# Performance work log

Hardware: AMD Instinct MI355X
Metric: run time of the kernel (lower is better)

## Reference

```python
import jax, jax.numpy as jnp
import numpy as np

LAYERS = [3, 1024, 512, 256, 128, 1]
WIDTHS = [3, 1024, 1024, 1024, 1024, 1]  # width per BsPINN: 2^(i-1)*Layers[i]
N = 131072


def _mask(num_blocks, bs1, bs2):
    # block-diagonal mask of ones, built statically (constant under jit)
    return jnp.asarray(np.kron(np.eye(num_blocks, dtype=np.float32),
                               np.ones((bs1, bs2), dtype=np.float32)))


def _xavier(key, shape, fan_in, fan_out):
    lim = np.sqrt(6.0 / (fan_in + fan_out)).astype(np.float32)
    return jax.random.uniform(key, shape, jnp.float32, -lim, lim)


def setup_inputs() -> dict:
    key = jax.random.key(0)
    ks = jax.random.split(key, 6)
    inp = {
        "X": jax.random.uniform(ks[0], (N, 3), dtype=jnp.float32),
        "lb_X": jnp.zeros((3,), jnp.float32),
        "ub_X": jnp.ones((3,), jnp.float32),
    }
    for i in range(5):
        # xavier scale per sub-block Layers[i] x Layers[i+1], as in the torch init
        inp[f"W{i}"] = _xavier(ks[i + 1], (WIDTHS[i], WIDTHS[i + 1]),
                               LAYERS[i], LAYERS[i + 1])
        inp[f"b{i}"] = jnp.zeros((1, WIDTHS[i + 1]), jnp.float32)
    return inp


def reference(X, lb_X, ub_X, W0, b0, W1, b1, W2, b2, W3, b3, W4, b4):
    # masks for hidden layers l=2,3: 2 blocks of 512x512, 4 blocks of 256x256
    m2 = _mask(2, LAYERS[2], 2 * LAYERS[3])   # [1024,1024]
    m3 = _mask(4, LAYERS[3], 2 * LAYERS[4])   # [1024,1024]
    h = 2.0 * (X - lb_X) / (ub_X - lb_X) - 1.0  # [N,3]
    h = jnp.sin(h @ W0 + b0)            # [N,1024] dense
    h = jnp.sin(h @ W1 + b1)            # [N,1024] dense
    h = jnp.sin(h @ (W2 * m2) + b2)     # [N,1024] block-diag (2 blocks)
    h = jnp.sin(h @ (W3 * m3) + b3)     # [N,1024] block-diag (4 blocks)
    return h @ W4 + b4                  # [N,1]
```

## Files before the change

### kernel.cpp

```cpp
#include <hip/hip_runtime.h>

typedef _Float16 f16x8 __attribute__((ext_vector_type(8)));
typedef _Float16 f16x4 __attribute__((ext_vector_type(4)));
typedef __fp16  fp16x2 __attribute__((ext_vector_type(2)));
typedef float f32x4 __attribute__((ext_vector_type(4)));
typedef unsigned int u32;

#define ROWS 64
#define THREADS 512

__global__ __launch_bounds__(512) void pack_weights(
    const float* __restrict__ W1, const float* __restrict__ W2,
    const float* __restrict__ W3, _Float16* __restrict__ WF1,
    _Float16* __restrict__ WF2, _Float16* __restrict__ WF3) {
  int t = blockIdx.x * 512 + threadIdx.x;
  const float* src; _Float16* dst; int idx, ct, kt, lane, kbase;
  if (t < 131072) {
    idx = t; src = W1; dst = WF1;
    ct = idx >> 11; kt = (idx >> 6) & 31; lane = idx & 63; kbase = 0;
  } else if (t < 196608) {
    idx = t - 131072; src = W2; dst = WF2;
    ct = idx >> 10; kt = (idx >> 6) & 15; lane = idx & 63;
    kbase = (ct >= 32) ? 512 : 0;
  } else {
    idx = t - 196608; src = W3; dst = WF3;
    ct = idx >> 9; kt = (idx >> 6) & 7; lane = idx & 63;
    kbase = (ct >> 4) << 8;
  }
  int c  = ct * 16 + (lane & 15);
  int k0 = kbase + kt * 32 + ((lane >> 4) << 3);
  f16x8 v;
#pragma unroll
  for (int j = 0; j < 8; ++j) v[j] = (_Float16)src[(size_t)(k0 + j) * 1024 + c];
  *reinterpret_cast<f16x8*>(dst + (size_t)idx * 8) = v;
}

template <int KT>
__device__ __forceinline__ void layer_mfma(char* hb, const _Float16* __restrict__ WF,
                                           const float* __restrict__ bias,
                                           int wid, int lane, int kbase) {
  f32x4 acc[8][4];
#pragma unroll
  for (int cf = 0; cf < 8; ++cf)
#pragma unroll
    for (int rf = 0; rf < 4; ++rf) acc[cf][rf] = f32x4{0.f, 0.f, 0.f, 0.f};

  const f16x8* wf = reinterpret_cast<const f16x8*>(WF) +
                    (u32)(wid * 8 * KT * 64 + lane);
  const int arow = lane & 15;
  const int koff = (lane >> 4) << 3;
  const u32 abase = (u32)(arow * 2048);
  const u32 axor  = (u32)((arow & 7) << 4);

  f16x8 wA[8], wB[8];
#define LOADW(buf, ktv)                                                        \
  { u32 _kt = (u32)(ktv);                                                      \
    _Pragma("unroll") for (int cf = 0; cf < 8; ++cf)                           \
      buf[cf] = wf[(u32)(cf * KT) * 64u + _kt * 64u]; }
#define DOMFMA(w, ktv)                                                         \
  { u32 kb = (u32)((kbase + (ktv) * 32 + koff) * 2);                           \
    f16x8 h[4];                                                                \
    _Pragma("unroll") for (int rf = 0; rf < 4; ++rf) {                         \
      u32 addr = ((u32)(rf * 32768) + abase + kb) ^ axor;                      \
      h[rf] = *reinterpret_cast<const f16x8*>(hb + addr);                      \
    }                                                                          \
    __builtin_amdgcn_s_setprio(1);                                             \
    _Pragma("unroll") for (int cf = 0; cf < 8; ++cf)                           \
      _Pragma("unroll") for (int rf = 0; rf < 4; ++rf)                         \
        acc[cf][rf] = __builtin_amdgcn_mfma_f32_16x16x32_f16(w[cf], h[rf],     \
                                                             acc[cf][rf], 0, 0, 0); \
    __builtin_amdgcn_s_setprio(0); }

  LOADW(wA, 0);
#pragma unroll 1
  for (int kt = 0; kt < KT; kt += 2) {
    int ktn = (kt + 2 < KT) ? (kt + 2) : 0;
    LOADW(wB, kt + 1);
    DOMFMA(wA, kt);
    LOADW(wA, ktn);
    DOMFMA(wB, kt + 1);
  }
#undef LOADW
#undef DOMFMA

  __syncthreads();
  const int csub = (lane >> 4) << 2;
  const int rr   = lane & 15;
#pragma unroll
  for (int cf = 0; cf < 8; ++cf) {
    int c0 = wid * 128 + cf * 16 + csub;
    f32x4 bb = *reinterpret_cast<const f32x4*>(bias + c0);
#pragma unroll
    for (int rf = 0; rf < 4; ++rf) {
      int r = rf * 16 + rr;
      float s0 = __sinf(acc[cf][rf][0] + bb[0]);
      float s1 = __sinf(acc[cf][rf][1] + bb[1]);
      float s2 = __sinf(acc[cf][rf][2] + bb[2]);
      float s3 = __sinf(acc[cf][rf][3] + bb[3]);
      union { fp16x2 h2[2]; f16x4 v; } pk;
      pk.h2[0] = __builtin_amdgcn_cvt_pkrtz(s0, s1);
      pk.h2[1] = __builtin_amdgcn_cvt_pkrtz(s2, s3);
      u32 addr = ((u32)(r * 2048 + c0 * 2)) ^ ((u32)((r & 7) << 4));
      *reinterpret_cast<f16x4*>(hb + addr) = pk.v;
    }
  }
  __syncthreads();
}

__global__
__attribute__((amdgpu_flat_work_group_size(512, 512), amdgpu_waves_per_eu(2, 2)))
void bspinn_fused(
    const float* __restrict__ X, const float* __restrict__ lb,
    const float* __restrict__ ub,
    const float* __restrict__ W0, const float* __restrict__ b0,
    const _Float16* __restrict__ WF1, const float* __restrict__ b1,
    const _Float16* __restrict__ WF2, const float* __restrict__ b2,
    const _Float16* __restrict__ WF3, const float* __restrict__ b3,
    const float* __restrict__ W4, const float* __restrict__ b4,
    float* __restrict__ out) {
  __shared__ alignas(16) char hb[ROWS * 2048];
  __shared__ float xs[ROWS * 4];
  __shared__ float partials[ROWS * 8];

  const int tid  = threadIdx.x;
  const int lane = tid & 63;
  const int wid  = tid >> 6;
  const int r0   = blockIdx.x * ROWS;

  if (tid < ROWS * 3) {
    int r = tid / 3, j = tid - r * 3;
    float x = X[(size_t)r0 * 3 + tid];
    xs[r * 4 + j] = 2.0f * (x - lb[j]) / (ub[j] - lb[j]) - 1.0f;
  }
  __syncthreads();

  {
    int c0 = tid * 2;
    float wa0 = W0[c0],        wb0 = W0[c0 + 1];
    float wa1 = W0[1024 + c0], wb1 = W0[1025 + c0];
    float wa2 = W0[2048 + c0], wb2 = W0[2049 + c0];
    float ba = b0[c0], bbv = b0[c0 + 1];
#pragma unroll 4
    for (int r = 0; r < ROWS; ++r) {
      float x0 = xs[r * 4], x1 = xs[r * 4 + 1], x2 = xs[r * 4 + 2];
      float va = __sinf(fmaf(x2, wa2, fmaf(x1, wa1, fmaf(x0, wa0, ba))));
      float vb = __sinf(fmaf(x2, wb2, fmaf(x1, wb1, fmaf(x0, wb0, bbv))));
      union { fp16x2 h2; u32 u; } pk;
      pk.h2 = __builtin_amdgcn_cvt_pkrtz(va, vb);
      u32 addr = ((u32)(r * 2048 + c0 * 2)) ^ ((u32)((r & 7) << 4));
      *reinterpret_cast<u32*>(hb + addr) = pk.u;
    }
  }
  __syncthreads();

  layer_mfma<32>(hb, WF1, b1, wid, lane, 0);
  layer_mfma<16>(hb, WF2, b2, wid, lane, (wid >> 2) * 512);
  layer_mfma<8 >(hb, WF3, b3, wid, lane, (wid >> 1) * 256);

  {
    int r = lane, seg = wid;
    u32 rb = (u32)(r * 2048);
    u32 xr = (u32)((r & 7) << 4);
    float s = 0.f;
#pragma unroll
    for (int kk = 0; kk < 128; kk += 8) {
      int k = seg * 128 + kk;
      f16x8 v = *reinterpret_cast<const f16x8*>(hb + ((rb + (u32)(k * 2)) ^ xr));
#pragma unroll
      for (int j = 0; j < 8; ++j) s = fmaf((float)v[j], W4[k + j], s);
    }
    partials[seg * 64 + r] = s;
  }
  __syncthreads();
  if (tid < ROWS) {
    float s = b4[0];
#pragma unroll
    for (int g = 0; g < 8; ++g) s += partials[g * 64 + tid];
    out[r0 + tid] = s;
  }
}

extern "C" void kernel_launch(void* const* d_in, const int* in_sizes, int n_in,
                              void* d_out, int out_size, void* d_ws, size_t ws_size,
                              hipStream_t stream) {
  const float* X  = (const float*)d_in[0];
  const float* lb = (const float*)d_in[1];
  const float* ub = (const float*)d_in[2];
  const float* W0 = (const float*)d_in[3];
  const float* b0 = (const float*)d_in[4];
  const float* W1 = (const float*)d_in[5];
  const float* b1 = (const float*)d_in[6];
  const float* W2 = (const float*)d_in[7];
  const float* b2 = (const float*)d_in[8];
  const float* W3 = (const float*)d_in[9];
  const float* b3 = (const float*)d_in[10];
  const float* W4 = (const float*)d_in[11];
  const float* b4 = (const float*)d_in[12];
  float* out = (float*)d_out;

  _Float16* WF1 = (_Float16*)d_ws;
  _Float16* WF2 = (_Float16*)((char*)d_ws + 2097152);
  _Float16* WF3 = (_Float16*)((char*)d_ws + 2097152 + 1048576);

  hipLaunchKernelGGL(pack_weights, dim3(448), dim3(512), 0, stream,
                     W1, W2, W3, WF1, WF2, WF3);
  hipLaunchKernelGGL(bspinn_fused, dim3(131072 / ROWS), dim3(THREADS), 0, stream,
                     X, lb, ub, W0, b0, WF1, b1, WF2, b2, WF3, b3, W4, b4, out);
}
```

Before: 482.8 us.

## Double workgroup to 1024 threads, halve per-wave column tiles, drop weight double-buffering

Each workgroup now runs 16 waves instead of 8. Each wave computes 64 output columns (4 column fragments) rather than 128, which halves accumulator and weight-register use and allows 4 waves per EU. The software double-buffered weight prefetch is replaced by a simple per-k-step load followed by MFMAs, relying on more resident waves to hide global-load latency. The layer-0 and final-reduction stages are re-split across the 1024 threads. In exchange, each LDS activation fragment now feeds only 4 column fragments instead of 8, so LDS reads per MFMA double, and explicit latency hiding of weight loads is lost.

```diff
diff --git a/kernel.cpp b/kernel.cpp
--- a/kernel.cpp
+++ b/kernel.cpp
@@ -7,7 +7,7 @@
 typedef unsigned int u32;
 
 #define ROWS 64
-#define THREADS 512
+#define THREADS 1024
 
 __global__ __launch_bounds__(512) void pack_weights(
     const float* __restrict__ W1, const float* __restrict__ W2,
@@ -39,56 +39,48 @@
 __device__ __forceinline__ void layer_mfma(char* hb, const _Float16* __restrict__ WF,
                                            const float* __restrict__ bias,
                                            int wid, int lane, int kbase) {
-  f32x4 acc[8][4];
+  f32x4 acc[4][4];
 #pragma unroll
-  for (int cf = 0; cf < 8; ++cf)
+  for (int cf = 0; cf < 4; ++cf)
 #pragma unroll
     for (int rf = 0; rf < 4; ++rf) acc[cf][rf] = f32x4{0.f, 0.f, 0.f, 0.f};
 
   const f16x8* wf = reinterpret_cast<const f16x8*>(WF) +
-                    (u32)(wid * 8 * KT * 64 + lane);
+                    (u32)(wid * 4 * KT * 64 + lane);
   const int arow = lane & 15;
   const int koff = (lane >> 4) << 3;
   const u32 abase = (u32)(arow * 2048);
   const u32 axor  = (u32)((arow & 7) << 4);
 
-  f16x8 wA[8], wB[8];
-#define LOADW(buf, ktv)                                                        \
-  { u32 _kt = (u32)(ktv);                                                      \
-    _Pragma("unroll") for (int cf = 0; cf < 8; ++cf)                           \
-      buf[cf] = wf[(u32)(cf * KT) * 64u + _kt * 64u]; }
-#define DOMFMA(w, ktv)                                                         \
-  { u32 kb = (u32)((kbase + (ktv) * 32 + koff) * 2);                           \
-    f16x8 h[4];                                                                \
-    _Pragma("unroll") for (int rf = 0; rf < 4; ++rf) {                         \
-      u32 addr = ((u32)(rf * 32768) + abase + kb) ^ axor;                      \
-      h[rf] = *reinterpret_cast<const f16x8*>(hb + addr);                      \
-    }                                                                          \
-    __builtin_amdgcn_s_setprio(1);                                             \
-    _Pragma("unroll") for (int cf = 0; cf < 8; ++cf)                           \
-      _Pragma("unroll") for (int rf = 0; rf < 4; ++rf)                         \
-        acc[cf][rf] = __builtin_amdgcn_mfma_f32_16x16x32_f16(w[cf], h[rf],     \
-                                                             acc[cf][rf], 0, 0, 0); \
-    __builtin_amdgcn_s_setprio(0); }
-
-  LOADW(wA, 0);
 #pragma unroll 1
-  for (int kt = 0; kt < KT; kt += 2) {
-    int ktn = (kt + 2 < KT) ? (kt + 2) : 0;
-    LOADW(wB, kt + 1);
-    DOMFMA(wA, kt);
-    LOADW(wA, ktn);
-    DOMFMA(wB, kt + 1);
+  for (int kt = 0; kt < KT; ++kt) {
+    f16x8 w[4];
+#pragma unroll
+    for (int cf = 0; cf < 4; ++cf)
+      w[cf] = wf[(u32)(cf * KT) * 64u + (u32)kt * 64u];
+    u32 kb = (u32)((kbase + kt * 32 + koff) * 2);
+    f16x8 h[4];
+#pragma unroll
+    for (int rf = 0; rf < 4; ++rf) {
+      u32 addr = ((u32)(rf * 32768) + abase + kb) ^ axor;
+      h[rf] = *reinterpret_cast<const f16x8*>(hb + addr);
+    }
+    __builtin_amdgcn_s_setprio(1);
+#pragma unroll
+    for (int cf = 0; cf < 4; ++cf)
+#pragma unroll
+      for (int rf = 0; rf < 4; ++rf)
+        acc[cf][rf] = __builtin_amdgcn_mfma_f32_16x16x32_f16(w[cf], h[rf],
+                                                             acc[cf][rf], 0, 0, 0);
+    __builtin_amdgcn_s_setprio(0);
   }
-#undef LOADW
-#undef DOMFMA
 
   __syncthreads();
   const int csub = (lane >> 4) << 2;
   const int rr   = lane & 15;
 #pragma unroll
-  for (int cf = 0; cf < 8; ++cf) {
-    int c0 = wid * 128 + cf * 16 + csub;
+  for (int cf = 0; cf < 4; ++cf) {
+    int c0 = wid * 64 + cf * 16 + csub;
     f32x4 bb = *reinterpret_cast<const f32x4*>(bias + c0);
 #pragma unroll
     for (int rf = 0; rf < 4; ++rf) {
@@ -108,7 +100,7 @@
 }
 
 __global__
-__attribute__((amdgpu_flat_work_group_size(512, 512), amdgpu_waves_per_eu(2, 2)))
+__attribute__((amdgpu_flat_work_group_size(1024, 1024), amdgpu_waves_per_eu(4, 4)))
 void bspinn_fused(
     const float* __restrict__ X, const float* __restrict__ lb,
     const float* __restrict__ ub,
@@ -120,7 +112,7 @@
     float* __restrict__ out) {
   __shared__ alignas(16) char hb[ROWS * 2048];
   __shared__ float xs[ROWS * 4];
-  __shared__ float partials[ROWS * 8];
+  __shared__ float partials[16 * ROWS];
 
   const int tid  = threadIdx.x;
   const int lane = tid & 63;
@@ -135,27 +127,24 @@
   __syncthreads();
 
   {
-    int c0 = tid * 2;
-    float wa0 = W0[c0],        wb0 = W0[c0 + 1];
-    float wa1 = W0[1024 + c0], wb1 = W0[1025 + c0];
-    float wa2 = W0[2048 + c0], wb2 = W0[2049 + c0];
-    float ba = b0[c0], bbv = b0[c0 + 1];
+    int c0 = tid;
+    float wa0 = W0[c0];
+    float wa1 = W0[1024 + c0];
+    float wa2 = W0[2048 + c0];
+    float ba = b0[c0];
 #pragma unroll 4
     for (int r = 0; r < ROWS; ++r) {
       float x0 = xs[r * 4], x1 = xs[r * 4 + 1], x2 = xs[r * 4 + 2];
       float va = __sinf(fmaf(x2, wa2, fmaf(x1, wa1, fmaf(x0, wa0, ba))));
-      float vb = __sinf(fmaf(x2, wb2, fmaf(x1, wb1, fmaf(x0, wb0, bbv))));
-      union { fp16x2 h2; u32 u; } pk;
-      pk.h2 = __builtin_amdgcn_cvt_pkrtz(va, vb);
       u32 addr = ((u32)(r * 2048 + c0 * 2)) ^ ((u32)((r & 7) << 4));
-      *reinterpret_cast<u32*>(hb + addr) = pk.u;
+      *reinterpret_cast<_Float16*>(hb + addr) = (_Float16)va;
     }
   }
   __syncthreads();
 
   layer_mfma<32>(hb, WF1, b1, wid, lane, 0);
-  layer_mfma<16>(hb, WF2, b2, wid, lane, (wid >> 2) * 512);
-  layer_mfma<8 >(hb, WF3, b3, wid, lane, (wid >> 1) * 256);
+  layer_mfma<16>(hb, WF2, b2, wid, lane, (wid >> 3) * 512);
+  layer_mfma<8 >(hb, WF3, b3, wid, lane, (wid >> 2) * 256);
 
   {
     int r = lane, seg = wid;
@@ -163,8 +152,8 @@
     u32 xr = (u32)((r & 7) << 4);
     float s = 0.f;
 #pragma unroll
-    for (int kk = 0; kk < 128; kk += 8) {
-      int k = seg * 128 + kk;
+    for (int kk = 0; kk < 64; kk += 8) {
+      int k = seg * 64 + kk;
       f16x8 v = *reinterpret_cast<const f16x8*>(hb + ((rb + (u32)(k * 2)) ^ xr));
 #pragma unroll
       for (int j = 0; j < 8; ++j) s = fmaf((float)v[j], W4[k + j], s);
@@ -175,7 +164,7 @@
   if (tid < ROWS) {
     float s = b4[0];
 #pragma unroll
-    for (int g = 0; g < 8; ++g) s += partials[g * 64 + tid];
+    for (int g = 0; g < 16; ++g) s += partials[g * 64 + tid];
     out[r0 + tid] = s;
   }
 }
```

After: 497.7 us. +3.1%, slower.
